# Kernel tuning notes

Measured on AMD Instinct MI355X. Metric: run time of the kernel, lower is better.

Reference implementation:

```python
import jax, jax.numpy as jnp
import numpy as np

U, N, L, C, D, B = 50000, 50000, 10, 256, 64, 4096


def setup_inputs() -> dict:
    key = jax.random.key(0)
    ks = jax.random.split(key, 12)
    xav = float(np.sqrt(6.0 / (D + D)))  # xavier_uniform bound for [D, D]
    return {
        "items": jax.random.randint(ks[0], (U, L), 0, N),
        "time_embs": jax.random.normal(ks[1], (U, L, D), dtype=jnp.float32),
        "user_embedding": jax.random.normal(ks[2], (U, D), dtype=jnp.float32),
        "item_embedding": jax.random.normal(ks[3], (N, D), dtype=jnp.float32),
        "cluster_emb": jax.random.normal(ks[4], (C, D), dtype=jnp.float32),
        "w_filters": jax.random.normal(ks[5], (U, L, D), dtype=jnp.float32),
        "Wq": jax.random.uniform(ks[6], (D, D), jnp.float32, -xav, xav),
        "Wk": jax.random.uniform(ks[7], (D, D), jnp.float32, -xav, xav),
        "Wv": jax.random.uniform(ks[8], (D, D), jnp.float32, -xav, xav),
        "users": jax.random.randint(ks[9], (B,), 0, U),
        "pos_items": jax.random.randint(ks[10], (B,), 0, N),
        "neg_items": jax.random.randint(ks[11], (B,), 0, N),
        "alpha1": jnp.float32(1.0),
        "alpha2": jnp.float32(1.0),
        "alpha3": jnp.float32(1.0),
    }


def reference(items, time_embs, user_embedding, item_embedding, cluster_emb,
              w_filters, Wq, Wk, Wv, users, pos_items, neg_items,
              alpha1, alpha2, alpha3):
    d = Wq.shape[0]
    # short_items_embs built under torch.no_grad / .detach() in the original
    short = jax.lax.stop_gradient(
        user_embedding[:, None, :] + item_embedding[items] + time_embs)  # [U,L,D]
    Q = short @ Wq                                   # [U,L,D]
    K = cluster_emb @ Wk                             # [C,D]
    V = cluster_emb @ Wv                             # [C,D]
    scores = jnp.einsum("uld,cd->ulc", Q, K) / jnp.sqrt(jnp.float32(d))
    attn = jax.nn.softmax(scores, axis=-1)           # [U,L,C]
    shorted = jnp.einsum("ulc,cd->uld", attn, V)     # [U,L,D]
    # matrix_filter = shorted^T @ w_filter per user -> [U,D,D]
    mfilt = jnp.einsum("uld,ule->ude", shorted, w_filters)
    new_user = jnp.einsum("ud,ude->ue", user_embedding, mfilt)  # [U,D]
    mix = alpha3 * (alpha1 * user_embedding + alpha2 * new_user)
    u_g = mix[users]                     # [B,D]
    pos_g = item_embedding[pos_items]    # [B,D]
    neg_g = item_embedding[neg_items]    # [B,D]
    return (u_g, pos_g, neg_g)
```

## Files before the change

### kernel.cpp

```cpp
#include <hip/hip_runtime.h>

#define D 64
#define L 10
#define C 256
#define G 8
#define SWB 72
#define ST 66

typedef __attribute__((ext_vector_type(8))) short bf16x8;
typedef __attribute__((ext_vector_type(4))) short short4v;
typedef __attribute__((ext_vector_type(4))) float f32x4;

__device__ inline short f2bf(float f) {
  unsigned u = __float_as_uint(f);
  u = (u + 0x7FFFu + ((u >> 16) & 1u)) >> 16;
  return (short)u;
}
__device__ inline float4 add3(float4 a, float4 b, float4 c) {
  return make_float4(a.x + b.x + c.x, a.y + b.y + c.y, a.z + b.z + c.z, a.w + b.w + c.w);
}
__device__ inline short4v f2bf4(float4 a) {
  short4v r;
  r[0] = f2bf(a.x); r[1] = f2bf(a.y); r[2] = f2bf(a.z); r[3] = f2bf(a.w);
  return r;
}

__global__ __launch_bounds__(256) void pre(const float* __restrict__ cl,
                                           const float* __restrict__ Wk,
                                           const float* __restrict__ Wq,
                                           const float* __restrict__ Wv,
                                           short* __restrict__ Bf) {
  __shared__ float s_cl[4 * 64];
  __shared__ float s_kc[4 * 64];
  __shared__ float s_w[64 * 65];
  const int t = threadIdx.x;
  const int bh = blockIdx.x >> 6, cb = blockIdx.x & 63;
  const int c0 = cb * 4;
  const int r = t >> 6, j = t & 63;

  s_cl[t] = cl[c0 * 64 + t];
  if (bh == 0) {
#pragma unroll
    for (int i = 0; i < 4; ++i) {
      int e = i * 256 + t;
      float4 v = ((const float4*)Wq)[e];
      int k = e >> 4, q = e & 15;
      float* dst = &s_w[k * 65 + q * 4];
      dst[0] = v.x; dst[1] = v.y; dst[2] = v.z; dst[3] = v.w;
    }
  }
  __syncthreads();

  const float* __restrict__ Wx = bh ? Wv : Wk;
  float acc = 0.f;
#pragma unroll 8
  for (int m = 0; m < 64; ++m) acc += s_cl[r * 64 + m] * Wx[m * 64 + j];

  if (bh == 1) {
    Bf[(c0 + r) * 128 + 64 + j] = f2bf(acc);
    return;
  }
  s_kc[t] = acc;
  __syncthreads();

  float o = 0.f;
#pragma unroll 8
  for (int jj = 0; jj < 64; ++jj) o += s_kc[r * 64 + jj] * s_w[j * 65 + jj];
  Bf[(c0 + r) * 128 + j] = f2bf(0.125f * o);
}

__device__ inline float reduce_row(const float2* __restrict__ rowp, int chunk) {
  float sx = 0.f, sy = 0.f;
#pragma unroll
  for (int j = 0; j < 8; ++j) {
    int jr = (j + chunk) & 7;
    float4 v = *(const float4*)&rowp[chunk * 16 + jr * 2];
    sx += v.x + v.z;
    sy += v.y + v.w;
  }
  sx += __shfl_xor(sx, 1, 64);
  sy += __shfl_xor(sy, 1, 64);
  sx += __shfl_xor(sx, 2, 64);
  sy += __shfl_xor(sy, 2, 64);
  return sy * __frcp_rn(sx);
}

__device__ inline float bcast(float v, int srclane) {
  return __uint_as_float(__builtin_amdgcn_readlane(__float_as_uint(v), srclane));
}

__global__ __launch_bounds__(256) void filter_main(
    const int* __restrict__ items, const float* __restrict__ te,
    const float* __restrict__ ue_g, const float* __restrict__ ie_g,
    const float* __restrict__ wf_g, const short* __restrict__ Bf,
    const int* __restrict__ users, const int* __restrict__ pos_items,
    const int* __restrict__ neg_items, const float* __restrict__ a1p,
    const float* __restrict__ a2p, const float* __restrict__ a3p,
    float* __restrict__ out, int B) {
  __shared__ short s_shb[88 * SWB];
  __shared__ float2 s2[80 * ST];

  const int tid = threadIdx.x, w = tid >> 6, lane = tid & 63;
  const int col16 = lane & 15, kb = lane >> 4;
  const int qr = col16 >> 2, jr = col16 & 3;
  const int b8 = blockIdx.x * G;
  const int BD = B * D;

  const int uA = users[b8 + w], uB = users[b8 + 4 + w];
  const float uevA = ue_g[uA * D + lane];
  const float uevB = ue_g[uB * D + lane];
  const float posvA = ie_g[pos_items[b8 + w] * D + lane];
  const float posvB = ie_g[pos_items[b8 + 4 + w] * D + lane];
  const float negvA = ie_g[neg_items[b8 + w] * D + lane];
  const float negvB = ie_g[neg_items[b8 + 4 + w] * D + lane];
  float wfvA[L], wfvB[L];
#pragma unroll
  for (int l = 0; l < L; ++l) {
    wfvA[l] = wf_g[(uA * L + l) * D + lane];
    wfvB[l] = wf_g[(uB * L + l) * D + lane];
  }

  {
    const float4* te4 = (const float4*)te;
    const float4* ie4 = (const float4*)ie_g;
    const float4* ue4 = (const float4*)ue_g;
    const int grp = tid >> 4, j = tid & 15;
#pragma unroll
    for (int it = 0; it < 6; ++it) {
      int row = it * 16 + grp;
      if (row < 80) {
        int g = row / 10, l = row - g * 10;
        int u = users[b8 + g];
        int itm = items[u * L + l];
        float4 v = add3(te4[(u * L + l) * 16 + j], ie4[itm * 16 + j],
                        ue4[u * 16 + j]);
        *(short4v*)&s_shb[row * SWB + j * 4] = f2bf4(v);
      } else if (row < 88) {
        int u = users[b8 + (row - 80)];
        *(short4v*)&s_shb[row * SWB + j * 4] = f2bf4(ue4[u * 16 + j]);
      }
    }
  }
  __syncthreads();

  bf16x8 af[6][2];
  bf16x8 au0, au1;
#pragma unroll
  for (int mt = 0; mt < 6; ++mt) {
    int g = 2 * qr + mt / 3;
    int l = (mt % 3) * 4 + jr;
    if (l < L) {
      const bf16x8* rp = (const bf16x8*)&s_shb[(g * 10 + l) * SWB];
      af[mt][0] = rp[kb];
      af[mt][1] = rp[4 + kb];
    } else {
      af[mt][0] = bf16x8{};
      af[mt][1] = bf16x8{};
    }
  }
  {
    const bf16x8* rp = (const bf16x8*)&s_shb[(80 + (col16 >> 1)) * SWB];
    au0 = rp[kb];
    au1 = rp[4 + kb];
  }

  float Sa[6][4], Ta[6][4];
#pragma unroll
  for (int mt = 0; mt < 6; ++mt)
#pragma unroll
    for (int jj = 0; jj < 4; ++jj) { Sa[mt][jj] = 0.f; Ta[mt][jj] = 0.f; }

#pragma unroll
  for (int nt = 0; nt < 4; ++nt) {
    const bf16x8* bp = (const bf16x8*)(Bf + ((w * 4 + nt) * 16 + col16) * 128);
    bf16x8 b0 = bp[kb], b1 = bp[4 + kb], b2 = bp[8 + kb], b3 = bp[12 + kb];
    f32x4 z = {0.f, 0.f, 0.f, 0.f};
    f32x4 cc[6];
    f32x4 cu = z;
#pragma unroll
    for (int mt = 0; mt < 6; ++mt) {
      cc[mt] = z;
      cc[mt] = __builtin_amdgcn_mfma_f32_16x16x32_bf16(af[mt][0], b0, cc[mt], 0, 0, 0);
      cc[mt] = __builtin_amdgcn_mfma_f32_16x16x32_bf16(af[mt][1], b1, cc[mt], 0, 0, 0);
    }
    cu = __builtin_amdgcn_mfma_f32_16x16x32_bf16(au0, b2, cu, 0, 0, 0);
    cu = __builtin_amdgcn_mfma_f32_16x16x32_bf16(au1, b3, cu, 0, 0, 0);
#pragma unroll
    for (int mt = 0; mt < 6; ++mt) {
      const float vuv = (mt < 3) ? cu[0] : cu[2];
#pragma unroll
      for (int jj = 0; jj < 4; ++jj) {
        if ((mt % 3) * 4 >= L && jj >= 2) continue;
        float e = __expf(cc[mt][jj]);
        Sa[mt][jj] += e;
        Ta[mt][jj] += e * vuv;
      }
    }
  }

#pragma unroll
  for (int mt = 0; mt < 6; ++mt)
#pragma unroll
    for (int jj = 0; jj < 4; ++jj) {
      const int l = (mt % 3) * 4 + jj;
      if (l < L) {
        int g = 2 * kb + mt / 3;
        s2[(g * 10 + l) * ST + w * 16 + col16] =
            make_float2(Sa[mt][jj], Ta[mt][jj]);
      }
    }
  __syncthreads();

  const int slot = lane >> 2, chunk = lane & 3;
  int rowA = (slot < 10) ? (w * 10 + slot) : ((w + 4) * 10 + (slot - 10));
  float slA_v = reduce_row(&s2[rowA * ST], chunk);
  int rowB = (slot < 4) ? ((w + 4) * 10 + 6 + slot) : 0;
  float slB_v = reduce_row(&s2[rowB * ST], chunk);

  float nuA = 0.f, nuB = 0.f;
#pragma unroll
  for (int l = 0; l < L; ++l) {
    nuA += bcast(slA_v, l * 4) * wfvA[l];
    float sb = (l < 6) ? bcast(slA_v, (10 + l) * 4) : bcast(slB_v, (l - 6) * 4);
    nuB += sb * wfvB[l];
  }

  const float a1 = *a1p, a2 = *a2p, a3 = *a3p;
  out[(b8 + w) * D + lane] = a3 * (a1 * uevA + a2 * nuA);
  out[(b8 + 4 + w) * D + lane] = a3 * (a1 * uevB + a2 * nuB);
  out[BD + (b8 + w) * D + lane] = posvA;
  out[BD + (b8 + 4 + w) * D + lane] = posvB;
  out[2 * BD + (b8 + w) * D + lane] = negvA;
  out[2 * BD + (b8 + 4 + w) * D + lane] = negvB;
}

extern "C" void kernel_launch(void* const* d_in, const int* in_sizes, int n_in,
                              void* d_out, int out_size, void* d_ws, size_t ws_size,
                              hipStream_t stream) {
  const int* items = (const int*)d_in[0];
  const float* time_embs = (const float*)d_in[1];
  const float* user_emb = (const float*)d_in[2];
  const float* item_emb = (const float*)d_in[3];
  const float* cluster = (const float*)d_in[4];
  const float* wf = (const float*)d_in[5];
  const float* Wq = (const float*)d_in[6];
  const float* Wk = (const float*)d_in[7];
  const float* Wv = (const float*)d_in[8];
  const int* users = (const int*)d_in[9];
  const int* pos = (const int*)d_in[10];
  const int* neg = (const int*)d_in[11];
  const float* a1 = (const float*)d_in[12];
  const float* a2 = (const float*)d_in[13];
  const float* a3 = (const float*)d_in[14];
  const int B = in_sizes[9];

  short* Bf = (short*)d_ws;
  hipLaunchKernelGGL(pre, dim3(128), dim3(256), 0, stream,
                     cluster, Wk, Wq, Wv, Bf);
  hipLaunchKernelGGL(filter_main, dim3(B / G), dim3(256), 0, stream,
                     items, time_embs, user_emb, item_emb, wf, Bf,
                     users, pos, neg, a1, a2, a3, (float*)d_out, B);
}
```

Baseline: 23.37 us.

## Split block work into two software-pipelined half-batches with double-buffered staging

Each block now handles two groups of 4 users instead of one group of 8. The gather and bf16 staging for the second group is issued into a second shared buffer while the MFMA/softmax work for the first group runs, so memory latency can overlap with compute. The cost is more barriers per block, a second pass over the Bf fragment loads, and half-filled MFMA tiles, since the user-vector tile now uses only cu[0].

```diff
diff --git a/kernel.cpp b/kernel.cpp
--- a/kernel.cpp
+++ b/kernel.cpp
@@ -3,7 +3,7 @@
 #define D 64
 #define L 10
 #define C 256
-#define G 8
+#define GPB 4
 #define SWB 72
 #define ST 66
 
@@ -96,142 +96,169 @@
     const int* __restrict__ users, const int* __restrict__ pos_items,
     const int* __restrict__ neg_items, const float* __restrict__ a1p,
     const float* __restrict__ a2p, const float* __restrict__ a3p,
-    float* __restrict__ out, int B) {
-  __shared__ short s_shb[88 * SWB];
-  __shared__ float2 s2[80 * ST];
+    float* __restrict__ out, int B, int NG) {
+  __shared__ short s_shb[2][44 * SWB];
+  __shared__ float2 s2[40 * ST];
 
   const int tid = threadIdx.x, w = tid >> 6, lane = tid & 63;
   const int col16 = lane & 15, kb = lane >> 4;
   const int qr = col16 >> 2, jr = col16 & 3;
-  const int b8 = blockIdx.x * G;
   const int BD = B * D;
 
-  const int uA = users[b8 + w], uB = users[b8 + 4 + w];
-  const float uevA = ue_g[uA * D + lane];
-  const float uevB = ue_g[uB * D + lane];
-  const float posvA = ie_g[pos_items[b8 + w] * D + lane];
-  const float posvB = ie_g[pos_items[b8 + 4 + w] * D + lane];
-  const float negvA = ie_g[neg_items[b8 + w] * D + lane];
-  const float negvB = ie_g[neg_items[b8 + 4 + w] * D + lane];
-  float wfvA[L], wfvB[L];
-#pragma unroll
-  for (int l = 0; l < L; ++l) {
-    wfvA[l] = wf_g[(uA * L + l) * D + lane];
-    wfvB[l] = wf_g[(uB * L + l) * D + lane];
-  }
+  const int base0 = blockIdx.x * GPB;
+  const int base1 = (blockIdx.x + NG) * GPB;
+
+#define STAGE(BUF, B4)                                                         \
+  {                                                                            \
+    const float4* te4 = (const float4*)te;                                     \
+    const float4* ie4 = (const float4*)ie_g;                                   \
+    const float4* ue4 = (const float4*)ue_g;                                   \
+    const int grp = tid >> 4, j = tid & 15;                                    \
+    _Pragma("unroll") for (int it = 0; it < 3; ++it) {                         \
+      int row = it * 16 + grp;                                                 \
+      if (row < 40) {                                                          \
+        int g = row / 10, l = row - g * 10;                                    \
+        int u = users[(B4) + g];                                               \
+        int itm = items[u * L + l];                                            \
+        float4 v = add3(te4[(u * L + l) * 16 + j], ie4[itm * 16 + j],          \
+                        ue4[u * 16 + j]);                                      \
+        *(short4v*)&(BUF)[row * SWB + j * 4] = f2bf4(v);                       \
+      } else if (row < 44) {                                                   \
+        int u = users[(B4) + (row - 40)];                                      \
+        *(short4v*)&(BUF)[row * SWB + j * 4] = f2bf4(ue4[u * 16 + j]);         \
+      }                                                                        \
+    }                                                                          \
+  }
+
+#define AFRAG(BUF, AF, AU0, AU1)                                               \
+  {                                                                            \
+    _Pragma("unroll") for (int mt = 0; mt < 3; ++mt) {                         \
+      int l = mt * 4 + jr;                                                     \
+      if (l < L) {                                                             \
+        const bf16x8* rp = (const bf16x8*)&(BUF)[(qr * 10 + l) * SWB];         \
+        AF[mt][0] = rp[kb];                                                    \
+        AF[mt][1] = rp[4 + kb];                                                \
+      } else {                                                                 \
+        AF[mt][0] = bf16x8{};                                                  \
+        AF[mt][1] = bf16x8{};                                                  \
+      }                                                                        \
+    }                                                                          \
+    const bf16x8* rp = (const bf16x8*)&(BUF)[(40 + qr) * SWB];                 \
+    AU0 = rp[kb];                                                              \
+    AU1 = rp[4 + kb];                                                          \
+  }
+
+#define COMPUTE(AF, AU0, AU1, SA, TA)                                          \
+  {                                                                            \
+    _Pragma("unroll") for (int mt = 0; mt < 3; ++mt)                           \
+        _Pragma("unroll") for (int jj = 0; jj < 4; ++jj) {                     \
+      SA[mt][jj] = 0.f;                                                        \
+      TA[mt][jj] = 0.f;                                                        \
+    }                                                                          \
+    _Pragma("unroll") for (int nt = 0; nt < 4; ++nt) {                         \
+      const bf16x8* bp =                                                       \
+          (const bf16x8*)(Bf + ((w * 4 + nt) * 16 + col16) * 128);             \
+      bf16x8 b0 = bp[kb], b1 = bp[4 + kb], b2 = bp[8 + kb], b3 = bp[12 + kb];  \
+      f32x4 z = {0.f, 0.f, 0.f, 0.f};                                          \
+      f32x4 cc[3];                                                             \
+      f32x4 cu = z;                                                            \
+      _Pragma("unroll") for (int mt = 0; mt < 3; ++mt) {                       \
+        cc[mt] = z;                                                            \
+        cc[mt] = __builtin_amdgcn_mfma_f32_16x16x32_bf16(AF[mt][0], b0,        \
+                                                         cc[mt], 0, 0, 0);     \
+        cc[mt] = __builtin_amdgcn_mfma_f32_16x16x32_bf16(AF[mt][1], b1,        \
+                                                         cc[mt], 0, 0, 0);     \
+      }                                                                        \
+      cu = __builtin_amdgcn_mfma_f32_16x16x32_bf16(AU0, b2, cu, 0, 0, 0);      \
+      cu = __builtin_amdgcn_mfma_f32_16x16x32_bf16(AU1, b3, cu, 0, 0, 0);      \
+      const float vuv = cu[0];     \
+      _Pragma("unroll") for (int mt = 0; mt < 3; ++mt)                         \
+          _Pragma("unroll") for (int jj = 0; jj < 4; ++jj) {                   \
+        if (mt * 4 + jj < L) {                                                 \
+          float e = __expf(cc[mt][jj]);                                        \
+          SA[mt][jj] += e;                                                     \
+          TA[mt][jj] += e * vuv;                                               \
+        }                                                                      \
+      }                                                                        \
+    }                                                                          \
+  }
+
+  STAGE(s_shb[0], base0)
+  const int u0 = users[base0 + w];
+  const float uev0 = ue_g[u0 * D + lane];
+  const float posv0 = ie_g[pos_items[base0 + w] * D + lane];
+  const float negv0 = ie_g[neg_items[base0 + w] * D + lane];
+  float wfv0[L];
+#pragma unroll
+  for (int l = 0; l < L; ++l) wfv0[l] = wf_g[(u0 * L + l) * D + lane];
+  __syncthreads();
+
+  bf16x8 af0[3][2], au00, au01;
+  AFRAG(s_shb[0], af0, au00, au01)
+  STAGE(s_shb[1], base1)
+  const int u1 = users[base1 + w];
+  const float uev1 = ue_g[u1 * D + lane];
+  const float posv1 = ie_g[pos_items[base1 + w] * D + lane];
+  const float negv1 = ie_g[neg_items[base1 + w] * D + lane];
+  float wfv1[L];
+#pragma unroll
+  for (int l = 0; l < L; ++l) wfv1[l] = wf_g[(u1 * L + l) * D + lane];
+
+  float Sa[3][4], Ta[3][4];
+  COMPUTE(af0, au00, au01, Sa, Ta)
+
+#pragma unroll
+  for (int mt = 0; mt < 3; ++mt)
+#pragma unroll
+    for (int jj = 0; jj < 4; ++jj) {
+      const int l = mt * 4 + jj;
+      if (l < L)
+        s2[(kb * 10 + l) * ST + w * 16 + col16] =
+            make_float2(Sa[mt][jj], Ta[mt][jj]);
+    }
+  __syncthreads();
 
   {
-    const float4* te4 = (const float4*)te;
-    const float4* ie4 = (const float4*)ie_g;
-    const float4* ue4 = (const float4*)ue_g;
-    const int grp = tid >> 4, j = tid & 15;
-#pragma unroll
-    for (int it = 0; it < 6; ++it) {
-      int row = it * 16 + grp;
-      if (row < 80) {
-        int g = row / 10, l = row - g * 10;
-        int u = users[b8 + g];
-        int itm = items[u * L + l];
-        float4 v = add3(te4[(u * L + l) * 16 + j], ie4[itm * 16 + j],
-                        ue4[u * 16 + j]);
-        *(short4v*)&s_shb[row * SWB + j * 4] = f2bf4(v);
-      } else if (row < 88) {
-        int u = users[b8 + (row - 80)];
-        *(short4v*)&s_shb[row * SWB + j * 4] = f2bf4(ue4[u * 16 + j]);
-      }
+    const int slot = lane >> 2, chunk = lane & 3;
+    int rowA = w * 10 + ((slot < 10) ? slot : 0);
+    float slv = reduce_row(&s2[rowA * ST], chunk);
+    float nu = 0.f;
+#pragma unroll
+    for (int l = 0; l < L; ++l) nu += bcast(slv, l * 4) * wfv0[l];
+    const float a1 = *a1p, a2 = *a2p, a3 = *a3p;
+    out[(base0 + w) * D + lane] = a3 * (a1 * uev0 + a2 * nu);
+    out[BD + (base0 + w) * D + lane] = posv0;
+    out[2 * BD + (base0 + w) * D + lane] = negv0;
+  }
+  __syncthreads();
+
+  bf16x8 af1[3][2], au10, au11;
+  AFRAG(s_shb[1], af1, au10, au11)
+  COMPUTE(af1, au10, au11, Sa, Ta)
+
+#pragma unroll
+  for (int mt = 0; mt < 3; ++mt)
+#pragma unroll
+    for (int jj = 0; jj < 4; ++jj) {
+      const int l = mt * 4 + jj;
+      if (l < L)
+        s2[(kb * 10 + l) * ST + w * 16 + col16] =
+            make_float2(Sa[mt][jj], Ta[mt][jj]);
     }
-  }
-  __syncthreads();
-
-  bf16x8 af[6][2];
-  bf16x8 au0, au1;
-#pragma unroll
-  for (int mt = 0; mt < 6; ++mt) {
-    int g = 2 * qr + mt / 3;
-    int l = (mt % 3) * 4 + jr;
-    if (l < L) {
-      const bf16x8* rp = (const bf16x8*)&s_shb[(g * 10 + l) * SWB];
-      af[mt][0] = rp[kb];
-      af[mt][1] = rp[4 + kb];
-    } else {
-      af[mt][0] = bf16x8{};
-      af[mt][1] = bf16x8{};
-    }
-  }
+  __syncthreads();
+
   {
-    const bf16x8* rp = (const bf16x8*)&s_shb[(80 + (col16 >> 1)) * SWB];
-    au0 = rp[kb];
-    au1 = rp[4 + kb];
-  }
-
-  float Sa[6][4], Ta[6][4];
-#pragma unroll
-  for (int mt = 0; mt < 6; ++mt)
-#pragma unroll
-    for (int jj = 0; jj < 4; ++jj) { Sa[mt][jj] = 0.f; Ta[mt][jj] = 0.f; }
-
-#pragma unroll
-  for (int nt = 0; nt < 4; ++nt) {
-    const bf16x8* bp = (const bf16x8*)(Bf + ((w * 4 + nt) * 16 + col16) * 128);
-    bf16x8 b0 = bp[kb], b1 = bp[4 + kb], b2 = bp[8 + kb], b3 = bp[12 + kb];
-    f32x4 z = {0.f, 0.f, 0.f, 0.f};
-    f32x4 cc[6];
-    f32x4 cu = z;
-#pragma unroll
-    for (int mt = 0; mt < 6; ++mt) {
-      cc[mt] = z;
-      cc[mt] = __builtin_amdgcn_mfma_f32_16x16x32_bf16(af[mt][0], b0, cc[mt], 0, 0, 0);
-      cc[mt] = __builtin_amdgcn_mfma_f32_16x16x32_bf16(af[mt][1], b1, cc[mt], 0, 0, 0);
-    }
-    cu = __builtin_amdgcn_mfma_f32_16x16x32_bf16(au0, b2, cu, 0, 0, 0);
-    cu = __builtin_amdgcn_mfma_f32_16x16x32_bf16(au1, b3, cu, 0, 0, 0);
-#pragma unroll
-    for (int mt = 0; mt < 6; ++mt) {
-      const float vuv = (mt < 3) ? cu[0] : cu[2];
-#pragma unroll
-      for (int jj = 0; jj < 4; ++jj) {
-        if ((mt % 3) * 4 >= L && jj >= 2) continue;
-        float e = __expf(cc[mt][jj]);
-        Sa[mt][jj] += e;
-        Ta[mt][jj] += e * vuv;
-      }
-    }
-  }
-
-#pragma unroll
-  for (int mt = 0; mt < 6; ++mt)
-#pragma unroll
-    for (int jj = 0; jj < 4; ++jj) {
-      const int l = (mt % 3) * 4 + jj;
-      if (l < L) {
-        int g = 2 * kb + mt / 3;
-        s2[(g * 10 + l) * ST + w * 16 + col16] =
-            make_float2(Sa[mt][jj], Ta[mt][jj]);
-      }
-    }
-  __syncthreads();
-
-  const int slot = lane >> 2, chunk = lane & 3;
-  int rowA = (slot < 10) ? (w * 10 + slot) : ((w + 4) * 10 + (slot - 10));
-  float slA_v = reduce_row(&s2[rowA * ST], chunk);
-  int rowB = (slot < 4) ? ((w + 4) * 10 + 6 + slot) : 0;
-  float slB_v = reduce_row(&s2[rowB * ST], chunk);
-
-  float nuA = 0.f, nuB = 0.f;
-#pragma unroll
-  for (int l = 0; l < L; ++l) {
-    nuA += bcast(slA_v, l * 4) * wfvA[l];
-    float sb = (l < 6) ? bcast(slA_v, (10 + l) * 4) : bcast(slB_v, (l - 6) * 4);
-    nuB += sb * wfvB[l];
-  }
-
-  const float a1 = *a1p, a2 = *a2p, a3 = *a3p;
-  out[(b8 + w) * D + lane] = a3 * (a1 * uevA + a2 * nuA);
-  out[(b8 + 4 + w) * D + lane] = a3 * (a1 * uevB + a2 * nuB);
-  out[BD + (b8 + w) * D + lane] = posvA;
-  out[BD + (b8 + 4 + w) * D + lane] = posvB;
-  out[2 * BD + (b8 + w) * D + lane] = negvA;
-  out[2 * BD + (b8 + 4 + w) * D + lane] = negvB;
+    const int slot = lane >> 2, chunk = lane & 3;
+    int rowA = w * 10 + ((slot < 10) ? slot : 0);
+    float slv = reduce_row(&s2[rowA * ST], chunk);
+    float nu = 0.f;
+#pragma unroll
+    for (int l = 0; l < L; ++l) nu += bcast(slv, l * 4) * wfv1[l];
+    const float a1 = *a1p, a2 = *a2p, a3 = *a3p;
+    out[(base1 + w) * D + lane] = a3 * (a1 * uev1 + a2 * nu);
+    out[BD + (base1 + w) * D + lane] = posv1;
+    out[2 * BD + (base1 + w) * D + lane] = negv1;
+  }
 }
 
 extern "C" void kernel_launch(void* const* d_in, const int* in_sizes, int n_in,
@@ -253,11 +280,12 @@
   const float* a2 = (const float*)d_in[13];
   const float* a3 = (const float*)d_in[14];
   const int B = in_sizes[9];
+  const int NG = B / GPB / 2;
 
   short* Bf = (short*)d_ws;
   hipLaunchKernelGGL(pre, dim3(128), dim3(256), 0, stream,
                      cluster, Wk, Wq, Wv, Bf);
-  hipLaunchKernelGGL(filter_main, dim3(B / G), dim3(256), 0, stream,
+  hipLaunchKernelGGL(filter_main, dim3(NG), dim3(256), 0, stream,
                      items, time_embs, user_emb, item_emb, wf, Bf,
-                     users, pos, neg, a1, a2, a3, (float*)d_out, B);
-}
+                     users, pos, neg, a1, a2, a3, (float*)d_out, B, NG);
+}
```

Result: slower. 26.07 us (+11.6%).

## Process four users per block instead of eight to double grid size

Applied to the files above, without the earlier changes.

Halves the number of users handled per workgroup (G from 8 to 4), so the grid grows from 512 to 1024 blocks on a GPU with many CUs. The MFMA tile mapping is rewritten so each 16-row tile covers four users times four positions with one user-vector row per quad, and the reduction and output stages are simplified to one user per wave. This raises parallelism and per-block latency hiding at the cost of reloading the shared cluster key/value fragments and repeating the exp work per block twice as often.

```diff
diff --git a/kernel.cpp b/kernel.cpp
--- a/kernel.cpp
+++ b/kernel.cpp
@@ -3,7 +3,7 @@
 #define D 64
 #define L 10
 #define C 256
-#define G 8
+#define G 4
 #define SWB 72
 #define ST 66
 
@@ -97,28 +97,22 @@
     const int* __restrict__ neg_items, const float* __restrict__ a1p,
     const float* __restrict__ a2p, const float* __restrict__ a3p,
     float* __restrict__ out, int B) {
-  __shared__ short s_shb[88 * SWB];
-  __shared__ float2 s2[80 * ST];
+  __shared__ short s_shb[44 * SWB];
+  __shared__ float2 s2[40 * ST];
 
   const int tid = threadIdx.x, w = tid >> 6, lane = tid & 63;
   const int col16 = lane & 15, kb = lane >> 4;
   const int qr = col16 >> 2, jr = col16 & 3;
-  const int b8 = blockIdx.x * G;
+  const int b4 = blockIdx.x * G;
   const int BD = B * D;
 
-  const int uA = users[b8 + w], uB = users[b8 + 4 + w];
+  const int uA = users[b4 + w];
   const float uevA = ue_g[uA * D + lane];
-  const float uevB = ue_g[uB * D + lane];
-  const float posvA = ie_g[pos_items[b8 + w] * D + lane];
-  const float posvB = ie_g[pos_items[b8 + 4 + w] * D + lane];
-  const float negvA = ie_g[neg_items[b8 + w] * D + lane];
-  const float negvB = ie_g[neg_items[b8 + 4 + w] * D + lane];
-  float wfvA[L], wfvB[L];
-#pragma unroll
-  for (int l = 0; l < L; ++l) {
-    wfvA[l] = wf_g[(uA * L + l) * D + lane];
-    wfvB[l] = wf_g[(uB * L + l) * D + lane];
-  }
+  const float posvA = ie_g[pos_items[b4 + w] * D + lane];
+  const float negvA = ie_g[neg_items[b4 + w] * D + lane];
+  float wfvA[L];
+#pragma unroll
+  for (int l = 0; l < L; ++l) wfvA[l] = wf_g[(uA * L + l) * D + lane];
 
   {
     const float4* te4 = (const float4*)te;
@@ -126,31 +120,30 @@
     const float4* ue4 = (const float4*)ue_g;
     const int grp = tid >> 4, j = tid & 15;
 #pragma unroll
-    for (int it = 0; it < 6; ++it) {
+    for (int it = 0; it < 3; ++it) {
       int row = it * 16 + grp;
-      if (row < 80) {
+      if (row < 40) {
         int g = row / 10, l = row - g * 10;
-        int u = users[b8 + g];
+        int u = users[b4 + g];
         int itm = items[u * L + l];
         float4 v = add3(te4[(u * L + l) * 16 + j], ie4[itm * 16 + j],
                         ue4[u * 16 + j]);
         *(short4v*)&s_shb[row * SWB + j * 4] = f2bf4(v);
-      } else if (row < 88) {
-        int u = users[b8 + (row - 80)];
+      } else if (row < 44) {
+        int u = users[b4 + (row - 40)];
         *(short4v*)&s_shb[row * SWB + j * 4] = f2bf4(ue4[u * 16 + j]);
       }
     }
   }
   __syncthreads();
 
-  bf16x8 af[6][2];
+  bf16x8 af[3][2];
   bf16x8 au0, au1;
 #pragma unroll
-  for (int mt = 0; mt < 6; ++mt) {
-    int g = 2 * qr + mt / 3;
-    int l = (mt % 3) * 4 + jr;
+  for (int mt = 0; mt < 3; ++mt) {
+    int l = mt * 4 + jr;
     if (l < L) {
-      const bf16x8* rp = (const bf16x8*)&s_shb[(g * 10 + l) * SWB];
+      const bf16x8* rp = (const bf16x8*)&s_shb[(qr * 10 + l) * SWB];
       af[mt][0] = rp[kb];
       af[mt][1] = rp[4 + kb];
     } else {
@@ -159,14 +152,14 @@
     }
   }
   {
-    const bf16x8* rp = (const bf16x8*)&s_shb[(80 + (col16 >> 1)) * SWB];
+    const bf16x8* rp = (const bf16x8*)&s_shb[(40 + qr) * SWB];
     au0 = rp[kb];
     au1 = rp[4 + kb];
   }
 
-  float Sa[6][4], Ta[6][4];
-#pragma unroll
-  for (int mt = 0; mt < 6; ++mt)
+  float Sa[3][4], Ta[3][4];
+#pragma unroll
+  for (int mt = 0; mt < 3; ++mt)
 #pragma unroll
     for (int jj = 0; jj < 4; ++jj) { Sa[mt][jj] = 0.f; Ta[mt][jj] = 0.f; }
 
@@ -175,63 +168,52 @@
     const bf16x8* bp = (const bf16x8*)(Bf + ((w * 4 + nt) * 16 + col16) * 128);
     bf16x8 b0 = bp[kb], b1 = bp[4 + kb], b2 = bp[8 + kb], b3 = bp[12 + kb];
     f32x4 z = {0.f, 0.f, 0.f, 0.f};
-    f32x4 cc[6];
+    f32x4 cc[3];
     f32x4 cu = z;
 #pragma unroll
-    for (int mt = 0; mt < 6; ++mt) {
+    for (int mt = 0; mt < 3; ++mt) {
       cc[mt] = z;
       cc[mt] = __builtin_amdgcn_mfma_f32_16x16x32_bf16(af[mt][0], b0, cc[mt], 0, 0, 0);
       cc[mt] = __builtin_amdgcn_mfma_f32_16x16x32_bf16(af[mt][1], b1, cc[mt], 0, 0, 0);
     }
     cu = __builtin_amdgcn_mfma_f32_16x16x32_bf16(au0, b2, cu, 0, 0, 0);
     cu = __builtin_amdgcn_mfma_f32_16x16x32_bf16(au1, b3, cu, 0, 0, 0);
-#pragma unroll
-    for (int mt = 0; mt < 6; ++mt) {
-      const float vuv = (mt < 3) ? cu[0] : cu[2];
+    const float vuv = cu[0];
+#pragma unroll
+    for (int mt = 0; mt < 3; ++mt)
 #pragma unroll
       for (int jj = 0; jj < 4; ++jj) {
-        if ((mt % 3) * 4 >= L && jj >= 2) continue;
-        float e = __expf(cc[mt][jj]);
-        Sa[mt][jj] += e;
-        Ta[mt][jj] += e * vuv;
+        if (mt * 4 + jj < L) {
+          float e = __expf(cc[mt][jj]);
+          Sa[mt][jj] += e;
+          Ta[mt][jj] += e * vuv;
+        }
       }
-    }
-  }
-
-#pragma unroll
-  for (int mt = 0; mt < 6; ++mt)
+  }
+
+#pragma unroll
+  for (int mt = 0; mt < 3; ++mt)
 #pragma unroll
     for (int jj = 0; jj < 4; ++jj) {
-      const int l = (mt % 3) * 4 + jj;
-      if (l < L) {
-        int g = 2 * kb + mt / 3;
-        s2[(g * 10 + l) * ST + w * 16 + col16] =
+      const int l = mt * 4 + jj;
+      if (l < L)
+        s2[(kb * 10 + l) * ST + w * 16 + col16] =
             make_float2(Sa[mt][jj], Ta[mt][jj]);
-      }
     }
   __syncthreads();
 
   const int slot = lane >> 2, chunk = lane & 3;
-  int rowA = (slot < 10) ? (w * 10 + slot) : ((w + 4) * 10 + (slot - 10));
-  float slA_v = reduce_row(&s2[rowA * ST], chunk);
-  int rowB = (slot < 4) ? ((w + 4) * 10 + 6 + slot) : 0;
-  float slB_v = reduce_row(&s2[rowB * ST], chunk);
-
-  float nuA = 0.f, nuB = 0.f;
-#pragma unroll
-  for (int l = 0; l < L; ++l) {
-    nuA += bcast(slA_v, l * 4) * wfvA[l];
-    float sb = (l < 6) ? bcast(slA_v, (10 + l) * 4) : bcast(slB_v, (l - 6) * 4);
-    nuB += sb * wfvB[l];
-  }
+  int rowA = w * 10 + ((slot < 10) ? slot : 0);
+  float slv = reduce_row(&s2[rowA * ST], chunk);
+
+  float nuA = 0.f;
+#pragma unroll
+  for (int l = 0; l < L; ++l) nuA += bcast(slv, l * 4) * wfvA[l];
 
   const float a1 = *a1p, a2 = *a2p, a3 = *a3p;
-  out[(b8 + w) * D + lane] = a3 * (a1 * uevA + a2 * nuA);
-  out[(b8 + 4 + w) * D + lane] = a3 * (a1 * uevB + a2 * nuB);
-  out[BD + (b8 + w) * D + lane] = posvA;
-  out[BD + (b8 + 4 + w) * D + lane] = posvB;
-  out[2 * BD + (b8 + w) * D + lane] = negvA;
-  out[2 * BD + (b8 + 4 + w) * D + lane] = negvB;
+  out[(b4 + w) * D + lane] = a3 * (a1 * uevA + a2 * nuA);
+  out[BD + (b4 + w) * D + lane] = posvA;
+  out[2 * BD + (b4 + w) * D + lane] = negvA;
 }
 
 extern "C" void kernel_launch(void* const* d_in, const int* in_sizes, int n_in,
```

Measured after the change: 28.35 us. +21.3%, slower.
